# Kernel optimization log

Measured on AMD Instinct MI355X. Metric: run time of the kernel, lower is better.

## Reference

```python
import jax, jax.numpy as jnp
import numpy as np

B, H, SQ, SK, D = 2, 16, 2048, 2048, 128
SCALE = 0.20884964425119185
P_DROP = 0.125

def setup_inputs() -> dict:
    key = jax.random.key(0)
    k1, k2, k3 = jax.random.split(key, 3)
    x1 = jax.random.normal(k1, (B, H, SQ, D), dtype=jnp.float32)
    x2 = jax.random.normal(k2, (B, H, SK, D), dtype=jnp.float32)
    # inverted dropout mask: 0 with prob p, else 1/(1-p)
    keep = jax.random.uniform(k3, (B, H, SQ, SK)) >= P_DROP
    dropout_mask = keep.astype(jnp.float32) / (1.0 - P_DROP)
    return {"x1": x1, "x2": x2, "dropout_mask": dropout_mask}

def reference(x1, x2, dropout_mask):
    # scores: [B,H,Sq,Sk]
    scores = jnp.einsum('bhqd,bhkd->bhqk', x1, x2) * SCALE
    attn = jax.nn.softmax(scores, axis=-1)
    attn = attn * dropout_mask
    # output: [B,H,Sq,D]
    return jnp.einsum('bhqk,bhkd->bhqd', attn, x2)
```

## Files before the change

kernel.cpp:

```cpp
#include <hip/hip_runtime.h>
#include <hip/hip_bf16.h>

#define SQ 2048
#define SK 2048
#define DD 128
#define NBH 32
#define QBLK 128
#define KBLK 32
#define NKT (SK / KBLK)
#define SCALE 0.20884964425119185f
#define SCL2 (SCALE * 1.4426950408889634f)

typedef __attribute__((ext_vector_type(8))) short short8;
typedef __attribute__((ext_vector_type(4))) float f32x4;

#define KPITCH 272
#define VPITCH 80
#define K0OFF 0
#define K1OFF 8704
#define V0OFF 17408
#define V1OFF 27648
#define SMEM_BYTES 37888

static __device__ __forceinline__ unsigned int pk_bf16(float lo, float hi) {
    float2 f2; f2.x = lo; f2.y = hi;
    __hip_bfloat162 h = __float22bfloat162_rn(f2);
    union { __hip_bfloat162 h2; unsigned int u; } cv; cv.h2 = h;
    return cv.u;
}

#define SOFTMAX_PACK(PA, SA_, SB_, MCa, MCb, LPART)                            \
  { float p_[8];                                                               \
    p_[0] = __builtin_amdgcn_exp2f(SA_[0]*SCL2);                               \
    p_[1] = __builtin_amdgcn_exp2f(SA_[1]*SCL2);                               \
    p_[2] = __builtin_amdgcn_exp2f(SA_[2]*SCL2);                               \
    p_[3] = __builtin_amdgcn_exp2f(SA_[3]*SCL2);                               \
    p_[4] = __builtin_amdgcn_exp2f(SB_[0]*SCL2);                               \
    p_[5] = __builtin_amdgcn_exp2f(SB_[1]*SCL2);                               \
    p_[6] = __builtin_amdgcn_exp2f(SB_[2]*SCL2);                               \
    p_[7] = __builtin_amdgcn_exp2f(SB_[3]*SCL2);                               \
    LPART += ((p_[0]+p_[1]) + (p_[2]+p_[3])) + ((p_[4]+p_[5]) + (p_[6]+p_[7]));\
    p_[0]*=MCa.x; p_[1]*=MCa.y; p_[2]*=MCa.z; p_[3]*=MCa.w;                    \
    p_[4]*=MCb.x; p_[5]*=MCb.y; p_[6]*=MCb.z; p_[7]*=MCb.w;                    \
    unsigned int P0 = pk_bf16(p_[0],p_[1]), P1 = pk_bf16(p_[2],p_[3]);         \
    unsigned int P2 = pk_bf16(p_[4],p_[5]), P3 = pk_bf16(p_[6],p_[7]);         \
    unsigned int a0 = __shfl((int)P0, sA), a2 = __shfl((int)P2, sA);           \
    unsigned int b0 = __shfl((int)P1, sA), b2 = __shfl((int)P3, sA);           \
    unsigned int c0 = __shfl((int)P0, sB), c2 = __shfl((int)P2, sB);           \
    unsigned int d0 = __shfl((int)P1, sB), d2 = __shfl((int)P3, sB);           \
    union { unsigned int u[4]; short8 v; } pb_;                                \
    pb_.u[0] = hi ? a2 : a0; pb_.u[1] = hi ? b2 : b0;                          \
    pb_.u[2] = hi ? c2 : c0; pb_.u[3] = hi ? d2 : d0;                          \
    PA = pb_.v; }

#define STAGE_SYNC()                                                           \
    asm volatile("s_waitcnt lgkmcnt(0)" ::: "memory");                         \
    __builtin_amdgcn_sched_barrier(0);                                         \
    __builtin_amdgcn_s_barrier();                 \
    __builtin_amdgcn_sched_barrier(0);

#define COMPUTE_TILE(KOFF_, VOFF_, MC0, MC1, MC2, MC3)                         \
    f32x4 s00={0,0,0,0}, s01={0,0,0,0}, s10={0,0,0,0}, s11={0,0,0,0};          \
    __builtin_amdgcn_s_setprio(1);                                             \
    _Pragma("unroll")                                                          \
    for (int ks = 0; ks < 4; ++ks) {                                           \
      short8 ka0 = *(const short8*)(smem + (KOFF_) + (c)      * KPITCH + ks*64 + 16*g); \
      short8 ka1 = *(const short8*)(smem + (KOFF_) + (16 + c) * KPITCH + ks*64 + 16*g); \
      s00 = __builtin_amdgcn_mfma_f32_16x16x32_bf16(ka0, qf0[ks], s00, 0,0,0); \
      s01 = __builtin_amdgcn_mfma_f32_16x16x32_bf16(ka1, qf0[ks], s01, 0,0,0); \
      s10 = __builtin_amdgcn_mfma_f32_16x16x32_bf16(ka0, qf1[ks], s10, 0,0,0); \
      s11 = __builtin_amdgcn_mfma_f32_16x16x32_bf16(ka1, qf1[ks], s11, 0,0,0); \
    }                                                                          \
    __builtin_amdgcn_s_setprio(0);                                             \
    short8 pa0, pa1;                                                           \
    SOFTMAX_PACK(pa0, s00, s01, MC0, MC1, l0p)                                 \
    SOFTMAX_PACK(pa1, s10, s11, MC2, MC3, l1p)                                 \
    __builtin_amdgcn_s_setprio(1);                                             \
    _Pragma("unroll")                                                          \
    for (int d8 = 0; d8 < 8; ++d8) {                                           \
      short8 vv = *(const short8*)(smem + (VOFF_) + (d8*16 + c)*VPITCH + 16*g);\
      o0[d8] = __builtin_amdgcn_mfma_f32_16x16x32_bf16(pa0, vv, o0[d8], 0,0,0);\
      o1[d8] = __builtin_amdgcn_mfma_f32_16x16x32_bf16(pa1, vv, o1[d8], 0,0,0);\
    }                                                                          \
    __builtin_amdgcn_s_setprio(0);

#define BODY_BF(KC0,KC1,VC0,VC1, MC0,MC1,MC2,MC3,                              \
                KN0,KN1,VN0,VN1, MN0,MN1,MN2,MN3, KOFF_, VOFF_, KT)            \
  { const int kbn = ((KT) < NKT - 1) ? ((KT) + 1) * KBLK : (KT) * KBLK;        \
    KN0 = *(const short8*)(x2bb + (size_t)(kbn + kk)      * DD + kd0);         \
    KN1 = *(const short8*)(x2bb + (size_t)(kbn + kk + 16) * DD + kd0);         \
    VN0 = *(const short8*)(x2bb + (size_t)(kbn + 2*kp)     * DD + vdb);        \
    VN1 = *(const short8*)(x2bb + (size_t)(kbn + 2*kp + 1) * DD + vdb);        \
    MN0 = *(const float4*)(mq0 + kbn);                                         \
    MN1 = *(const float4*)(mq0 + kbn + 16);                                    \
    MN2 = *(const float4*)(mq1 + kbn);                                         \
    MN3 = *(const float4*)(mq1 + kbn + 16);                                    \
    *(short8*)(smem + (KOFF_) + (kk)      * KPITCH + 2*kd0) = KC0;             \
    *(short8*)(smem + (KOFF_) + (kk + 16) * KPITCH + 2*kd0) = KC1;             \
    { union { short8 s; unsigned int u[4]; } a_, b_;                           \
      a_.s = VC0; b_.s = VC1;                                                  \
      _Pragma("unroll")                                                        \
      for (int j = 0; j < 8; ++j) {                                            \
        unsigned int w = (j & 1)                                               \
            ? ((a_.u[j>>1] >> 16) | (b_.u[j>>1] & 0xffff0000u))                \
            : ((a_.u[j>>1] & 0xffffu) | (b_.u[j>>1] << 16));                   \
        *(unsigned int*)(smem + (VOFF_) + (vdb + j) * VPITCH + 4*kp) = w;      \
      } }                                                                      \
    STAGE_SYNC()                                                               \
    COMPUTE_TILE(KOFF_, VOFF_, MC0, MC1, MC2, MC3)                             \
  }

#define BODY_F32(KC0,KC1,KC2,KC3, VC0,VC1,VC2,VC3, MC0,MC1,MC2,MC3,            \
                 KN0,KN1,KN2,KN3, VN0,VN1,VN2,VN3, MN0,MN1,MN2,MN3,            \
                 KOFF_, VOFF_, KT)                                             \
  { const int kbn = ((KT) < NKT - 1) ? ((KT) + 1) * KBLK : (KT) * KBLK;        \
    KN0 = *(const float4*)(x2fb + (size_t)(kbn + kk)      * DD + kd0);         \
    KN1 = *(const float4*)(x2fb + (size_t)(kbn + kk)      * DD + kd0 + 4);     \
    KN2 = *(const float4*)(x2fb + (size_t)(kbn + kk + 16) * DD + kd0);         \
    KN3 = *(const float4*)(x2fb + (size_t)(kbn + kk + 16) * DD + kd0 + 4);     \
    VN0 = *(const float4*)(x2fb + (size_t)(kbn + 2*kp)     * DD + vdb);        \
    VN1 = *(const float4*)(x2fb + (size_t)(kbn + 2*kp)     * DD + vdb + 4);    \
    VN2 = *(const float4*)(x2fb + (size_t)(kbn + 2*kp + 1) * DD + vdb);        \
    VN3 = *(const float4*)(x2fb + (size_t)(kbn + 2*kp + 1) * DD + vdb + 4);    \
    MN0 = *(const float4*)(mq0 + kbn);                                         \
    MN1 = *(const float4*)(mq0 + kbn + 16);                                    \
    MN2 = *(const float4*)(mq1 + kbn);                                         \
    MN3 = *(const float4*)(mq1 + kbn + 16);                                    \
    { union { unsigned int u[4]; short8 s; } k0_, k1_;                         \
      k0_.u[0]=pk_bf16(KC0.x,KC0.y); k0_.u[1]=pk_bf16(KC0.z,KC0.w);            \
      k0_.u[2]=pk_bf16(KC1.x,KC1.y); k0_.u[3]=pk_bf16(KC1.z,KC1.w);            \
      k1_.u[0]=pk_bf16(KC2.x,KC2.y); k1_.u[1]=pk_bf16(KC2.z,KC2.w);            \
      k1_.u[2]=pk_bf16(KC3.x,KC3.y); k1_.u[3]=pk_bf16(KC3.z,KC3.w);            \
      *(short8*)(smem + (KOFF_) + (kk)      * KPITCH + 2*kd0) = k0_.s;         \
      *(short8*)(smem + (KOFF_) + (kk + 16) * KPITCH + 2*kd0) = k1_.s; }       \
    *(unsigned int*)(smem + (VOFF_) + (vdb+0)*VPITCH + 4*kp) = pk_bf16(VC0.x, VC2.x); \
    *(unsigned int*)(smem + (VOFF_) + (vdb+1)*VPITCH + 4*kp) = pk_bf16(VC0.y, VC2.y); \
    *(unsigned int*)(smem + (VOFF_) + (vdb+2)*VPITCH + 4*kp) = pk_bf16(VC0.z, VC2.z); \
    *(unsigned int*)(smem + (VOFF_) + (vdb+3)*VPITCH + 4*kp) = pk_bf16(VC0.w, VC2.w); \
    *(unsigned int*)(smem + (VOFF_) + (vdb+4)*VPITCH + 4*kp) = pk_bf16(VC1.x, VC3.x); \
    *(unsigned int*)(smem + (VOFF_) + (vdb+5)*VPITCH + 4*kp) = pk_bf16(VC1.y, VC3.y); \
    *(unsigned int*)(smem + (VOFF_) + (vdb+6)*VPITCH + 4*kp) = pk_bf16(VC1.z, VC3.z); \
    *(unsigned int*)(smem + (VOFF_) + (vdb+7)*VPITCH + 4*kp) = pk_bf16(VC1.w, VC3.w); \
    STAGE_SYNC()                                                               \
    COMPUTE_TILE(KOFF_, VOFF_, MC0, MC1, MC2, MC3)                             \
  }

#define KERNEL_PRE()                                                           \
    __shared__ __align__(16) unsigned char smem[SMEM_BYTES];                   \
    const int tid  = threadIdx.x;                                              \
    const int lane = tid & 63, wid = tid >> 6;                                 \
    const int c = lane & 15, g = lane >> 4;                                    \
    const int bid = blockIdx.x;                                                \
    const int swz = (bid & 7) * 64 + (bid >> 3);   \
    const int bh = swz >> 4;                                                   \
    const int qb = swz & 15;                                                   \
    const float* x1b = x1 + ((size_t)bh * SQ + (size_t)qb * QBLK) * DD;        \
    const float* mb  = mask + ((size_t)bh * SQ + (size_t)qb * QBLK) * SK;      \
    float*      outb = out + ((size_t)bh * SQ + (size_t)qb * QBLK) * DD;       \
    const int sA = c + ((g & 1) << 5);                                         \
    const int sB = sA + 16;                                                    \
    const bool hi = (g >= 2);                                                  \
    const int kk  = tid >> 4, kd0 = (tid & 15) * 8;                            \
    const int kp  = tid & 15, vdb = (tid >> 4) * 8;                            \
    const float* mq0 = mb + (size_t)(wid*16 + c) * SK + 4*g;                   \
    const float* mq1 = mq0 + (size_t)64 * SK;

#define KERNEL_QLOAD()                                                         \
    short8 qf0[4], qf1[4];                                                     \
    {  const float* q0r = x1b + (size_t)(wid*16 + c) * DD;                     \
       const float* q1r = q0r + (size_t)64 * DD;                               \
       _Pragma("unroll")                                                       \
       for (int ks = 0; ks < 4; ++ks) {                                        \
           float4 a = *(const float4*)(q0r + ks*32 + 8*g);                     \
           float4 b = *(const float4*)(q0r + ks*32 + 8*g + 4);                 \
           union { unsigned int u[4]; short8 s; } t;                           \
           t.u[0]=pk_bf16(a.x,a.y); t.u[1]=pk_bf16(a.z,a.w);                   \
           t.u[2]=pk_bf16(b.x,b.y); t.u[3]=pk_bf16(b.z,b.w);                   \
           qf0[ks]=t.s;                                                        \
           a = *(const float4*)(q1r + ks*32 + 8*g);                            \
           b = *(const float4*)(q1r + ks*32 + 8*g + 4);                        \
           t.u[0]=pk_bf16(a.x,a.y); t.u[1]=pk_bf16(a.z,a.w);                   \
           t.u[2]=pk_bf16(b.x,b.y); t.u[3]=pk_bf16(b.z,b.w);                   \
           qf1[ks]=t.s;                                                        \
       } }

#define KERNEL_EPILOGUE()                                                      \
    float l0 = l0p; l0 += __shfl_xor(l0, 16); l0 += __shfl_xor(l0, 32);        \
    float l1 = l1p; l1 += __shfl_xor(l1, 16); l1 += __shfl_xor(l1, 32);        \
    float il00 = 1.0f/__shfl(l0, 4*g+0), il01 = 1.0f/__shfl(l0, 4*g+1);        \
    float il02 = 1.0f/__shfl(l0, 4*g+2), il03 = 1.0f/__shfl(l0, 4*g+3);        \
    float il10 = 1.0f/__shfl(l1, 4*g+0), il11 = 1.0f/__shfl(l1, 4*g+1);        \
    float il12 = 1.0f/__shfl(l1, 4*g+2), il13 = 1.0f/__shfl(l1, 4*g+3);        \
    float* orow0 = outb + (size_t)(wid*16) * DD;                               \
    float* orow1 = outb + (size_t)(64 + wid*16) * DD;                          \
    _Pragma("unroll")                                                          \
    for (int d8 = 0; d8 < 8; ++d8) {                                           \
        orow0[(4*g + 0) * DD + d8*16 + c] = o0[d8][0] * il00;                  \
        orow0[(4*g + 1) * DD + d8*16 + c] = o0[d8][1] * il01;                  \
        orow0[(4*g + 2) * DD + d8*16 + c] = o0[d8][2] * il02;                  \
        orow0[(4*g + 3) * DD + d8*16 + c] = o0[d8][3] * il03;                  \
        orow1[(4*g + 0) * DD + d8*16 + c] = o1[d8][0] * il10;                  \
        orow1[(4*g + 1) * DD + d8*16 + c] = o1[d8][1] * il11;                  \
        orow1[(4*g + 2) * DD + d8*16 + c] = o1[d8][2] * il12;                  \
        orow1[(4*g + 3) * DD + d8*16 + c] = o1[d8][3] * il13;                  \
    }

__global__ __launch_bounds__(256) void cvt_x2(const float* __restrict__ src,
                                              unsigned short* __restrict__ dst,
                                              int n4) {
    int i = blockIdx.x * 256 + threadIdx.x;
    const int stride = gridDim.x * 256;
    for (; i < n4; i += stride) {
        float4 v = ((const float4*)src)[i];
        uint2 w; w.x = pk_bf16(v.x, v.y); w.y = pk_bf16(v.z, v.w);
        ((uint2*)dst)[i] = w;
    }
}

__global__ __launch_bounds__(256, 2) void fattn_bf16(
    const float* __restrict__ x1, const unsigned short* __restrict__ x2b,
    const float* __restrict__ mask, float* __restrict__ out)
{
    KERNEL_PRE()
    const unsigned short* x2bb = x2b + (size_t)bh * SK * DD;

    short8 kA0 = *(const short8*)(x2bb + (size_t)(kk)      * DD + kd0);
    short8 kA1 = *(const short8*)(x2bb + (size_t)(kk + 16) * DD + kd0);
    short8 vA0 = *(const short8*)(x2bb + (size_t)(2*kp)     * DD + vdb);
    short8 vA1 = *(const short8*)(x2bb + (size_t)(2*kp + 1) * DD + vdb);
    float4 mA0 = *(const float4*)(mq0);
    float4 mA1 = *(const float4*)(mq0 + 16);
    float4 mA2 = *(const float4*)(mq1);
    float4 mA3 = *(const float4*)(mq1 + 16);
    short8 kB0, kB1, vB0, vB1; float4 mB0, mB1, mB2, mB3;

    KERNEL_QLOAD()

    f32x4 o0[8] = {}, o1[8] = {};
    float l0p = 0.f, l1p = 0.f;

    for (int kt2 = 0; kt2 < NKT / 2; ++kt2) {
        BODY_BF(kA0,kA1,vA0,vA1, mA0,mA1,mA2,mA3,
                kB0,kB1,vB0,vB1, mB0,mB1,mB2,mB3, K0OFF, V0OFF, 2*kt2)
        BODY_BF(kB0,kB1,vB0,vB1, mB0,mB1,mB2,mB3,
                kA0,kA1,vA0,vA1, mA0,mA1,mA2,mA3, K1OFF, V1OFF, 2*kt2 + 1)
    }
    KERNEL_EPILOGUE()
}

__global__ __launch_bounds__(256, 2) void fattn_f32(
    const float* __restrict__ x1, const float* __restrict__ x2,
    const float* __restrict__ mask, float* __restrict__ out)
{
    KERNEL_PRE()
    const float* x2fb = x2 + (size_t)bh * SK * DD;

    float4 kA0 = *(const float4*)(x2fb + (size_t)(kk)      * DD + kd0);
    float4 kA1 = *(const float4*)(x2fb + (size_t)(kk)      * DD + kd0 + 4);
    float4 kA2 = *(const float4*)(x2fb + (size_t)(kk + 16) * DD + kd0);
    float4 kA3 = *(const float4*)(x2fb + (size_t)(kk + 16) * DD + kd0 + 4);
    float4 vA0 = *(const float4*)(x2fb + (size_t)(2*kp)     * DD + vdb);
    float4 vA1 = *(const float4*)(x2fb + (size_t)(2*kp)     * DD + vdb + 4);
    float4 vA2 = *(const float4*)(x2fb + (size_t)(2*kp + 1) * DD + vdb);
    float4 vA3 = *(const float4*)(x2fb + (size_t)(2*kp + 1) * DD + vdb + 4);
    float4 mA0 = *(const float4*)(mq0);
    float4 mA1 = *(const float4*)(mq0 + 16);
    float4 mA2 = *(const float4*)(mq1);
    float4 mA3 = *(const float4*)(mq1 + 16);
    float4 kB0,kB1,kB2,kB3, vB0,vB1,vB2,vB3, mB0,mB1,mB2,mB3;

    KERNEL_QLOAD()

    f32x4 o0[8] = {}, o1[8] = {};
    float l0p = 0.f, l1p = 0.f;

    for (int kt2 = 0; kt2 < NKT / 2; ++kt2) {
        BODY_F32(kA0,kA1,kA2,kA3, vA0,vA1,vA2,vA3, mA0,mA1,mA2,mA3,
                 kB0,kB1,kB2,kB3, vB0,vB1,vB2,vB3, mB0,mB1,mB2,mB3,
                 K0OFF, V0OFF, 2*kt2)
        BODY_F32(kB0,kB1,kB2,kB3, vB0,vB1,vB2,vB3, mB0,mB1,mB2,mB3,
                 kA0,kA1,kA2,kA3, vA0,vA1,vA2,vA3, mA0,mA1,mA2,mA3,
                 K1OFF, V1OFF, 2*kt2 + 1)
    }
    KERNEL_EPILOGUE()
}

extern "C" void kernel_launch(void* const* d_in, const int* in_sizes, int n_in,
                              void* d_out, int out_size, void* d_ws, size_t ws_size,
                              hipStream_t stream) {
    const float* x1   = (const float*)d_in[0];
    const float* x2   = (const float*)d_in[1];
    const float* mask = (const float*)d_in[2];
    float* out = (float*)d_out;
    const size_t need = (size_t)NBH * SK * DD * sizeof(unsigned short);
    if (ws_size >= need) {
        unsigned short* x2b = (unsigned short*)d_ws;
        cvt_x2<<<dim3(2048), dim3(256), 0, stream>>>(x2, x2b, NBH*SK*DD/4);
        fattn_bf16<<<dim3(NBH * (SQ / QBLK)), dim3(256), 0, stream>>>(x1, x2b, mask, out);
    } else {
        fattn_f32<<<dim3(NBH * (SQ / QBLK)), dim3(256), 0, stream>>>(x1, x2, mask, out);
    }
}
```

Before: 223.2 us.

## Restructure bf16 attention loop to compute current tile before staging next to LDS

The bf16 path now issues global loads for the next K/V tile, computes QK^T, softmax and PV from the already-staged LDS buffer, then writes the next tile into the alternate LDS buffer and synchronises once. This lets the global load latency overlap the MFMA work, and it issues dropout mask loads two tiles ahead. The first tile is staged in a prologue before the loop. The PV loop is also reordered to load two V fragments per iteration. The f32 fallback is rewritten to use a single buffer with two barriers per tile. Register pressure rises from holding prefetched data across the compute.

```diff
diff --git a/kernel.cpp b/kernel.cpp
--- a/kernel.cpp
+++ b/kernel.cpp
@@ -53,96 +53,69 @@
     pb_.u[2] = hi ? c2 : c0; pb_.u[3] = hi ? d2 : d0;                          \
     PA = pb_.v; }
 
-#define STAGE_SYNC()                                                           \
+#define BAR()                                                                  \
     asm volatile("s_waitcnt lgkmcnt(0)" ::: "memory");                         \
     __builtin_amdgcn_sched_barrier(0);                                         \
-    __builtin_amdgcn_s_barrier();                 \
+    __builtin_amdgcn_s_barrier();                                              \
     __builtin_amdgcn_sched_barrier(0);
 
-#define COMPUTE_TILE(KOFF_, VOFF_, MC0, MC1, MC2, MC3)                         \
+#define BODY_BF(KOFFc, VOFFc, KOFFn, VOFFn, MC0, MC1, MC2, MC3, KT)            \
+  {                                                                            \
+    const int kbn = (((KT) < NKT - 1) ? (KT) + 1 : (KT)) * KBLK;               \
+    const int kbm = (((KT) < NKT - 2) ? (KT) + 2 : (NKT - 1)) * KBLK;          \
+                   \
+    kC0 = *(const short8*)(x2bb + (size_t)(kbn + kk)      * DD + kd0);         \
+    kC1 = *(const short8*)(x2bb + (size_t)(kbn + kk + 16) * DD + kd0);         \
+    vC0 = *(const short8*)(x2bb + (size_t)(kbn + 2*kp)     * DD + vdb);        \
+    vC1 = *(const short8*)(x2bb + (size_t)(kbn + 2*kp + 1) * DD + vdb);        \
+                                                \
     f32x4 s00={0,0,0,0}, s01={0,0,0,0}, s10={0,0,0,0}, s11={0,0,0,0};          \
     __builtin_amdgcn_s_setprio(1);                                             \
     _Pragma("unroll")                                                          \
     for (int ks = 0; ks < 4; ++ks) {                                           \
-      short8 ka0 = *(const short8*)(smem + (KOFF_) + (c)      * KPITCH + ks*64 + 16*g); \
-      short8 ka1 = *(const short8*)(smem + (KOFF_) + (16 + c) * KPITCH + ks*64 + 16*g); \
+      short8 ka0 = *(const short8*)(smem + (KOFFc) + (c)      * KPITCH + ks*64 + 16*g); \
+      short8 ka1 = *(const short8*)(smem + (KOFFc) + (16 + c) * KPITCH + ks*64 + 16*g); \
       s00 = __builtin_amdgcn_mfma_f32_16x16x32_bf16(ka0, qf0[ks], s00, 0,0,0); \
       s01 = __builtin_amdgcn_mfma_f32_16x16x32_bf16(ka1, qf0[ks], s01, 0,0,0); \
       s10 = __builtin_amdgcn_mfma_f32_16x16x32_bf16(ka0, qf1[ks], s10, 0,0,0); \
       s11 = __builtin_amdgcn_mfma_f32_16x16x32_bf16(ka1, qf1[ks], s11, 0,0,0); \
     }                                                                          \
     __builtin_amdgcn_s_setprio(0);                                             \
+                                     \
     short8 pa0, pa1;                                                           \
     SOFTMAX_PACK(pa0, s00, s01, MC0, MC1, l0p)                                 \
     SOFTMAX_PACK(pa1, s10, s11, MC2, MC3, l1p)                                 \
+                                                \
     __builtin_amdgcn_s_setprio(1);                                             \
     _Pragma("unroll")                                                          \
-    for (int d8 = 0; d8 < 8; ++d8) {                                           \
-      short8 vv = *(const short8*)(smem + (VOFF_) + (d8*16 + c)*VPITCH + 16*g);\
-      o0[d8] = __builtin_amdgcn_mfma_f32_16x16x32_bf16(pa0, vv, o0[d8], 0,0,0);\
-      o1[d8] = __builtin_amdgcn_mfma_f32_16x16x32_bf16(pa1, vv, o1[d8], 0,0,0);\
+    for (int d4 = 0; d4 < 4; ++d4) {                                           \
+      short8 v0 = *(const short8*)(smem + (VOFFc) + ((2*d4)*16   + c)*VPITCH + 16*g); \
+      short8 v1 = *(const short8*)(smem + (VOFFc) + ((2*d4+1)*16 + c)*VPITCH + 16*g); \
+      o0[2*d4]   = __builtin_amdgcn_mfma_f32_16x16x32_bf16(pa0, v0, o0[2*d4],   0,0,0); \
+      o1[2*d4]   = __builtin_amdgcn_mfma_f32_16x16x32_bf16(pa1, v0, o1[2*d4],   0,0,0); \
+      o0[2*d4+1] = __builtin_amdgcn_mfma_f32_16x16x32_bf16(pa0, v1, o0[2*d4+1], 0,0,0); \
+      o1[2*d4+1] = __builtin_amdgcn_mfma_f32_16x16x32_bf16(pa1, v1, o1[2*d4+1], 0,0,0); \
     }                                                                          \
-    __builtin_amdgcn_s_setprio(0);
-
-#define BODY_BF(KC0,KC1,VC0,VC1, MC0,MC1,MC2,MC3,                              \
-                KN0,KN1,VN0,VN1, MN0,MN1,MN2,MN3, KOFF_, VOFF_, KT)            \
-  { const int kbn = ((KT) < NKT - 1) ? ((KT) + 1) * KBLK : (KT) * KBLK;        \
-    KN0 = *(const short8*)(x2bb + (size_t)(kbn + kk)      * DD + kd0);         \
-    KN1 = *(const short8*)(x2bb + (size_t)(kbn + kk + 16) * DD + kd0);         \
-    VN0 = *(const short8*)(x2bb + (size_t)(kbn + 2*kp)     * DD + vdb);        \
-    VN1 = *(const short8*)(x2bb + (size_t)(kbn + 2*kp + 1) * DD + vdb);        \
-    MN0 = *(const float4*)(mq0 + kbn);                                         \
-    MN1 = *(const float4*)(mq0 + kbn + 16);                                    \
-    MN2 = *(const float4*)(mq1 + kbn);                                         \
-    MN3 = *(const float4*)(mq1 + kbn + 16);                                    \
-    *(short8*)(smem + (KOFF_) + (kk)      * KPITCH + 2*kd0) = KC0;             \
-    *(short8*)(smem + (KOFF_) + (kk + 16) * KPITCH + 2*kd0) = KC1;             \
+    __builtin_amdgcn_s_setprio(0);                                             \
+     \
+    *(short8*)(smem + (KOFFn) + (kk)      * KPITCH + 2*kd0) = kC0;             \
+    *(short8*)(smem + (KOFFn) + (kk + 16) * KPITCH + 2*kd0) = kC1;             \
     { union { short8 s; unsigned int u[4]; } a_, b_;                           \
-      a_.s = VC0; b_.s = VC1;                                                  \
+      a_.s = vC0; b_.s = vC1;                                                  \
       _Pragma("unroll")                                                        \
       for (int j = 0; j < 8; ++j) {                                            \
         unsigned int w = (j & 1)                                               \
             ? ((a_.u[j>>1] >> 16) | (b_.u[j>>1] & 0xffff0000u))                \
             : ((a_.u[j>>1] & 0xffffu) | (b_.u[j>>1] << 16));                   \
-        *(unsigned int*)(smem + (VOFF_) + (vdb + j) * VPITCH + 4*kp) = w;      \
+        *(unsigned int*)(smem + (VOFFn) + (vdb + j) * VPITCH + 4*kp) = w;      \
       } }                                                                      \
-    STAGE_SYNC()                                                               \
-    COMPUTE_TILE(KOFF_, VOFF_, MC0, MC1, MC2, MC3)                             \
-  }
-
-#define BODY_F32(KC0,KC1,KC2,KC3, VC0,VC1,VC2,VC3, MC0,MC1,MC2,MC3,            \
-                 KN0,KN1,KN2,KN3, VN0,VN1,VN2,VN3, MN0,MN1,MN2,MN3,            \
-                 KOFF_, VOFF_, KT)                                             \
-  { const int kbn = ((KT) < NKT - 1) ? ((KT) + 1) * KBLK : (KT) * KBLK;        \
-    KN0 = *(const float4*)(x2fb + (size_t)(kbn + kk)      * DD + kd0);         \
-    KN1 = *(const float4*)(x2fb + (size_t)(kbn + kk)      * DD + kd0 + 4);     \
-    KN2 = *(const float4*)(x2fb + (size_t)(kbn + kk + 16) * DD + kd0);         \
-    KN3 = *(const float4*)(x2fb + (size_t)(kbn + kk + 16) * DD + kd0 + 4);     \
-    VN0 = *(const float4*)(x2fb + (size_t)(kbn + 2*kp)     * DD + vdb);        \
-    VN1 = *(const float4*)(x2fb + (size_t)(kbn + 2*kp)     * DD + vdb + 4);    \
-    VN2 = *(const float4*)(x2fb + (size_t)(kbn + 2*kp + 1) * DD + vdb);        \
-    VN3 = *(const float4*)(x2fb + (size_t)(kbn + 2*kp + 1) * DD + vdb + 4);    \
-    MN0 = *(const float4*)(mq0 + kbn);                                         \
-    MN1 = *(const float4*)(mq0 + kbn + 16);                                    \
-    MN2 = *(const float4*)(mq1 + kbn);                                         \
-    MN3 = *(const float4*)(mq1 + kbn + 16);                                    \
-    { union { unsigned int u[4]; short8 s; } k0_, k1_;                         \
-      k0_.u[0]=pk_bf16(KC0.x,KC0.y); k0_.u[1]=pk_bf16(KC0.z,KC0.w);            \
-      k0_.u[2]=pk_bf16(KC1.x,KC1.y); k0_.u[3]=pk_bf16(KC1.z,KC1.w);            \
-      k1_.u[0]=pk_bf16(KC2.x,KC2.y); k1_.u[1]=pk_bf16(KC2.z,KC2.w);            \
-      k1_.u[2]=pk_bf16(KC3.x,KC3.y); k1_.u[3]=pk_bf16(KC3.z,KC3.w);            \
-      *(short8*)(smem + (KOFF_) + (kk)      * KPITCH + 2*kd0) = k0_.s;         \
-      *(short8*)(smem + (KOFF_) + (kk + 16) * KPITCH + 2*kd0) = k1_.s; }       \
-    *(unsigned int*)(smem + (VOFF_) + (vdb+0)*VPITCH + 4*kp) = pk_bf16(VC0.x, VC2.x); \
-    *(unsigned int*)(smem + (VOFF_) + (vdb+1)*VPITCH + 4*kp) = pk_bf16(VC0.y, VC2.y); \
-    *(unsigned int*)(smem + (VOFF_) + (vdb+2)*VPITCH + 4*kp) = pk_bf16(VC0.z, VC2.z); \
-    *(unsigned int*)(smem + (VOFF_) + (vdb+3)*VPITCH + 4*kp) = pk_bf16(VC0.w, VC2.w); \
-    *(unsigned int*)(smem + (VOFF_) + (vdb+4)*VPITCH + 4*kp) = pk_bf16(VC1.x, VC3.x); \
-    *(unsigned int*)(smem + (VOFF_) + (vdb+5)*VPITCH + 4*kp) = pk_bf16(VC1.y, VC3.y); \
-    *(unsigned int*)(smem + (VOFF_) + (vdb+6)*VPITCH + 4*kp) = pk_bf16(VC1.z, VC3.z); \
-    *(unsigned int*)(smem + (VOFF_) + (vdb+7)*VPITCH + 4*kp) = pk_bf16(VC1.w, VC3.w); \
-    STAGE_SYNC()                                                               \
-    COMPUTE_TILE(KOFF_, VOFF_, MC0, MC1, MC2, MC3)                             \
+    \
+    MC0 = *(const float4*)(mq0 + kbm);                                         \
+    MC1 = *(const float4*)(mq0 + kbm + 16);                                    \
+    MC2 = *(const float4*)(mq1 + kbm);                                         \
+    MC3 = *(const float4*)(mq1 + kbm + 16);                                    \
+                                       \
+    BAR()                                                                      \
   }
 
 #define KERNEL_PRE()                                                           \
@@ -224,29 +197,102 @@
     KERNEL_PRE()
     const unsigned short* x2bb = x2b + (size_t)bh * SK * DD;
 
-    short8 kA0 = *(const short8*)(x2bb + (size_t)(kk)      * DD + kd0);
-    short8 kA1 = *(const short8*)(x2bb + (size_t)(kk + 16) * DD + kd0);
-    short8 vA0 = *(const short8*)(x2bb + (size_t)(2*kp)     * DD + vdb);
-    short8 vA1 = *(const short8*)(x2bb + (size_t)(2*kp + 1) * DD + vdb);
+    short8 kC0 = *(const short8*)(x2bb + (size_t)(kk)      * DD + kd0);
+    short8 kC1 = *(const short8*)(x2bb + (size_t)(kk + 16) * DD + kd0);
+    short8 vC0 = *(const short8*)(x2bb + (size_t)(2*kp)     * DD + vdb);
+    short8 vC1 = *(const short8*)(x2bb + (size_t)(2*kp + 1) * DD + vdb);
     float4 mA0 = *(const float4*)(mq0);
     float4 mA1 = *(const float4*)(mq0 + 16);
     float4 mA2 = *(const float4*)(mq1);
     float4 mA3 = *(const float4*)(mq1 + 16);
-    short8 kB0, kB1, vB0, vB1; float4 mB0, mB1, mB2, mB3;
+    float4 mB0 = *(const float4*)(mq0 + KBLK);
+    float4 mB1 = *(const float4*)(mq0 + KBLK + 16);
+    float4 mB2 = *(const float4*)(mq1 + KBLK);
+    float4 mB3 = *(const float4*)(mq1 + KBLK + 16);
 
     KERNEL_QLOAD()
+
+    *(short8*)(smem + K0OFF + (kk)      * KPITCH + 2*kd0) = kC0;
+    *(short8*)(smem + K0OFF + (kk + 16) * KPITCH + 2*kd0) = kC1;
+    { union { short8 s; unsigned int u[4]; } a_, b_;
+      a_.s = vC0; b_.s = vC1;
+#pragma unroll
+      for (int j = 0; j < 8; ++j) {
+        unsigned int w = (j & 1)
+            ? ((a_.u[j>>1] >> 16) | (b_.u[j>>1] & 0xffff0000u))
+            : ((a_.u[j>>1] & 0xffffu) | (b_.u[j>>1] << 16));
+        *(unsigned int*)(smem + V0OFF + (vdb + j) * VPITCH + 4*kp) = w;
+      } }
+    BAR()
 
     f32x4 o0[8] = {}, o1[8] = {};
     float l0p = 0.f, l1p = 0.f;
 
     for (int kt2 = 0; kt2 < NKT / 2; ++kt2) {
-        BODY_BF(kA0,kA1,vA0,vA1, mA0,mA1,mA2,mA3,
-                kB0,kB1,vB0,vB1, mB0,mB1,mB2,mB3, K0OFF, V0OFF, 2*kt2)
-        BODY_BF(kB0,kB1,vB0,vB1, mB0,mB1,mB2,mB3,
-                kA0,kA1,vA0,vA1, mA0,mA1,mA2,mA3, K1OFF, V1OFF, 2*kt2 + 1)
+        BODY_BF(K0OFF, V0OFF, K1OFF, V1OFF, mA0, mA1, mA2, mA3, 2*kt2)
+        BODY_BF(K1OFF, V1OFF, K0OFF, V0OFF, mB0, mB1, mB2, mB3, 2*kt2 + 1)
     }
     KERNEL_EPILOGUE()
 }
+
+#define F32_SYNC()                                                             \
+    asm volatile("s_waitcnt lgkmcnt(0)" ::: "memory");                         \
+    __builtin_amdgcn_sched_barrier(0);                                         \
+    __builtin_amdgcn_s_barrier();                                              \
+    __builtin_amdgcn_sched_barrier(0);
+
+#define BODY_F32(KC0,KC1,KC2,KC3, VC0,VC1,VC2,VC3, MC0,MC1,MC2,MC3,            \
+                 KN0,KN1,KN2,KN3, VN0,VN1,VN2,VN3, MN0,MN1,MN2,MN3, KT)        \
+  { const int kbn = ((KT) < NKT - 1) ? ((KT) + 1) * KBLK : (KT) * KBLK;        \
+    KN0 = *(const float4*)(x2fb + (size_t)(kbn + kk)      * DD + kd0);         \
+    KN1 = *(const float4*)(x2fb + (size_t)(kbn + kk)      * DD + kd0 + 4);     \
+    KN2 = *(const float4*)(x2fb + (size_t)(kbn + kk + 16) * DD + kd0);         \
+    KN3 = *(const float4*)(x2fb + (size_t)(kbn + kk + 16) * DD + kd0 + 4);     \
+    VN0 = *(const float4*)(x2fb + (size_t)(kbn + 2*kp)     * DD + vdb);        \
+    VN1 = *(const float4*)(x2fb + (size_t)(kbn + 2*kp)     * DD + vdb + 4);    \
+    VN2 = *(const float4*)(x2fb + (size_t)(kbn + 2*kp + 1) * DD + vdb);        \
+    VN3 = *(const float4*)(x2fb + (size_t)(kbn + 2*kp + 1) * DD + vdb + 4);    \
+    MN0 = *(const float4*)(mq0 + kbn);                                         \
+    MN1 = *(const float4*)(mq0 + kbn + 16);                                    \
+    MN2 = *(const float4*)(mq1 + kbn);                                         \
+    MN3 = *(const float4*)(mq1 + kbn + 16);                                    \
+    { union { unsigned int u[4]; short8 s; } k0_, k1_;                         \
+      k0_.u[0]=pk_bf16(KC0.x,KC0.y); k0_.u[1]=pk_bf16(KC0.z,KC0.w);            \
+      k0_.u[2]=pk_bf16(KC1.x,KC1.y); k0_.u[3]=pk_bf16(KC1.z,KC1.w);            \
+      k1_.u[0]=pk_bf16(KC2.x,KC2.y); k1_.u[1]=pk_bf16(KC2.z,KC2.w);            \
+      k1_.u[2]=pk_bf16(KC3.x,KC3.y); k1_.u[3]=pk_bf16(KC3.z,KC3.w);            \
+      *(short8*)(smem + K0OFF + (kk)      * KPITCH + 2*kd0) = k0_.s;           \
+      *(short8*)(smem + K0OFF + (kk + 16) * KPITCH + 2*kd0) = k1_.s; }         \
+    *(unsigned int*)(smem + V0OFF + (vdb+0)*VPITCH + 4*kp) = pk_bf16(VC0.x, VC2.x); \
+    *(unsigned int*)(smem + V0OFF + (vdb+1)*VPITCH + 4*kp) = pk_bf16(VC0.y, VC2.y); \
+    *(unsigned int*)(smem + V0OFF + (vdb+2)*VPITCH + 4*kp) = pk_bf16(VC0.z, VC2.z); \
+    *(unsigned int*)(smem + V0OFF + (vdb+3)*VPITCH + 4*kp) = pk_bf16(VC0.w, VC2.w); \
+    *(unsigned int*)(smem + V0OFF + (vdb+4)*VPITCH + 4*kp) = pk_bf16(VC1.x, VC3.x); \
+    *(unsigned int*)(smem + V0OFF + (vdb+5)*VPITCH + 4*kp) = pk_bf16(VC1.y, VC3.y); \
+    *(unsigned int*)(smem + V0OFF + (vdb+6)*VPITCH + 4*kp) = pk_bf16(VC1.z, VC3.z); \
+    *(unsigned int*)(smem + V0OFF + (vdb+7)*VPITCH + 4*kp) = pk_bf16(VC1.w, VC3.w); \
+    F32_SYNC()                                                                 \
+    f32x4 s00={0,0,0,0}, s01={0,0,0,0}, s10={0,0,0,0}, s11={0,0,0,0};          \
+    _Pragma("unroll")                                                          \
+    for (int ks = 0; ks < 4; ++ks) {                                           \
+      short8 ka0 = *(const short8*)(smem + K0OFF + (c)      * KPITCH + ks*64 + 16*g); \
+      short8 ka1 = *(const short8*)(smem + K0OFF + (16 + c) * KPITCH + ks*64 + 16*g); \
+      s00 = __builtin_amdgcn_mfma_f32_16x16x32_bf16(ka0, qf0[ks], s00, 0,0,0); \
+      s01 = __builtin_amdgcn_mfma_f32_16x16x32_bf16(ka1, qf0[ks], s01, 0,0,0); \
+      s10 = __builtin_amdgcn_mfma_f32_16x16x32_bf16(ka0, qf1[ks], s10, 0,0,0); \
+      s11 = __builtin_amdgcn_mfma_f32_16x16x32_bf16(ka1, qf1[ks], s11, 0,0,0); \
+    }                                                                          \
+    short8 pa0, pa1;                                                           \
+    SOFTMAX_PACK(pa0, s00, s01, MC0, MC1, l0p)                                 \
+    SOFTMAX_PACK(pa1, s10, s11, MC2, MC3, l1p)                                 \
+    _Pragma("unroll")                                                          \
+    for (int d8 = 0; d8 < 8; ++d8) {                                           \
+      short8 vv = *(const short8*)(smem + V0OFF + (d8*16 + c)*VPITCH + 16*g);  \
+      o0[d8] = __builtin_amdgcn_mfma_f32_16x16x32_bf16(pa0, vv, o0[d8], 0,0,0);\
+      o1[d8] = __builtin_amdgcn_mfma_f32_16x16x32_bf16(pa1, vv, o1[d8], 0,0,0);\
+    }                                                                          \
+    F32_SYNC()                                                                 \
+  }
 
 __global__ __launch_bounds__(256, 2) void fattn_f32(
     const float* __restrict__ x1, const float* __restrict__ x2,
@@ -276,11 +322,9 @@
 
     for (int kt2 = 0; kt2 < NKT / 2; ++kt2) {
         BODY_F32(kA0,kA1,kA2,kA3, vA0,vA1,vA2,vA3, mA0,mA1,mA2,mA3,
-                 kB0,kB1,kB2,kB3, vB0,vB1,vB2,vB3, mB0,mB1,mB2,mB3,
-                 K0OFF, V0OFF, 2*kt2)
+                 kB0,kB1,kB2,kB3, vB0,vB1,vB2,vB3, mB0,mB1,mB2,mB3, 2*kt2)
         BODY_F32(kB0,kB1,kB2,kB3, vB0,vB1,vB2,vB3, mB0,mB1,mB2,mB3,
-                 kA0,kA1,kA2,kA3, vA0,vA1,vA2,vA3, mA0,mA1,mA2,mA3,
-                 K1OFF, V1OFF, 2*kt2 + 1)
+                 kA0,kA1,kA2,kA3, vA0,vA1,vA2,vA3, mA0,mA1,mA2,mA3, 2*kt2 + 1)
     }
     KERNEL_EPILOGUE()
 }
```

Result: faster. 210.5 us (-5.7%).

## Halve query tile to 64 rows, single-buffer LDS, raise occupancy

Applied to the files above, without the earlier changes.

Each block now processes 64 query rows instead of 128, so every wave owns one 16-row slice. The double-buffered K/V LDS staging becomes a single buffer with a second barrier after compute, which halves shared memory. Launch bounds rise to 4 blocks per CU for the bf16 kernel and 3 for the f32 fallback, and the grid doubles. The goal is more occupancy and better latency hiding of the mask stream. In exchange, K/V is reloaded from global memory twice as often per query row, each tile costs an extra barrier, and each wave does less MFMA work per K/V tile.

```diff
diff --git a/kernel.cpp b/kernel.cpp
--- a/kernel.cpp
+++ b/kernel.cpp
@@ -5,7 +5,7 @@
 #define SK 2048
 #define DD 128
 #define NBH 32
-#define QBLK 128
+#define QBLK 64
 #define KBLK 32
 #define NKT (SK / KBLK)
 #define SCALE 0.20884964425119185f
@@ -16,11 +16,8 @@
 
 #define KPITCH 272
 #define VPITCH 80
-#define K0OFF 0
-#define K1OFF 8704
-#define V0OFF 17408
-#define V1OFF 27648
-#define SMEM_BYTES 37888
+#define VOFF 8704
+#define SMEM_BYTES 18944
 
 static __device__ __forceinline__ unsigned int pk_bf16(float lo, float hi) {
     float2 f2; f2.x = lo; f2.y = hi;
@@ -53,39 +50,13 @@
     pb_.u[2] = hi ? c2 : c0; pb_.u[3] = hi ? d2 : d0;                          \
     PA = pb_.v; }
 
-#define STAGE_SYNC()                                                           \
+#define BAR()                                                                  \
     asm volatile("s_waitcnt lgkmcnt(0)" ::: "memory");                         \
     __builtin_amdgcn_sched_barrier(0);                                         \
-    __builtin_amdgcn_s_barrier();                 \
+    __builtin_amdgcn_s_barrier();                                              \
     __builtin_amdgcn_sched_barrier(0);
 
-#define COMPUTE_TILE(KOFF_, VOFF_, MC0, MC1, MC2, MC3)                         \
-    f32x4 s00={0,0,0,0}, s01={0,0,0,0}, s10={0,0,0,0}, s11={0,0,0,0};          \
-    __builtin_amdgcn_s_setprio(1);                                             \
-    _Pragma("unroll")                                                          \
-    for (int ks = 0; ks < 4; ++ks) {                                           \
-      short8 ka0 = *(const short8*)(smem + (KOFF_) + (c)      * KPITCH + ks*64 + 16*g); \
-      short8 ka1 = *(const short8*)(smem + (KOFF_) + (16 + c) * KPITCH + ks*64 + 16*g); \
-      s00 = __builtin_amdgcn_mfma_f32_16x16x32_bf16(ka0, qf0[ks], s00, 0,0,0); \
-      s01 = __builtin_amdgcn_mfma_f32_16x16x32_bf16(ka1, qf0[ks], s01, 0,0,0); \
-      s10 = __builtin_amdgcn_mfma_f32_16x16x32_bf16(ka0, qf1[ks], s10, 0,0,0); \
-      s11 = __builtin_amdgcn_mfma_f32_16x16x32_bf16(ka1, qf1[ks], s11, 0,0,0); \
-    }                                                                          \
-    __builtin_amdgcn_s_setprio(0);                                             \
-    short8 pa0, pa1;                                                           \
-    SOFTMAX_PACK(pa0, s00, s01, MC0, MC1, l0p)                                 \
-    SOFTMAX_PACK(pa1, s10, s11, MC2, MC3, l1p)                                 \
-    __builtin_amdgcn_s_setprio(1);                                             \
-    _Pragma("unroll")                                                          \
-    for (int d8 = 0; d8 < 8; ++d8) {                                           \
-      short8 vv = *(const short8*)(smem + (VOFF_) + (d8*16 + c)*VPITCH + 16*g);\
-      o0[d8] = __builtin_amdgcn_mfma_f32_16x16x32_bf16(pa0, vv, o0[d8], 0,0,0);\
-      o1[d8] = __builtin_amdgcn_mfma_f32_16x16x32_bf16(pa1, vv, o1[d8], 0,0,0);\
-    }                                                                          \
-    __builtin_amdgcn_s_setprio(0);
-
-#define BODY_BF(KC0,KC1,VC0,VC1, MC0,MC1,MC2,MC3,                              \
-                KN0,KN1,VN0,VN1, MN0,MN1,MN2,MN3, KOFF_, VOFF_, KT)            \
+#define BODY_BF(KC0,KC1,VC0,VC1, MC0,MC1, KN0,KN1,VN0,VN1, MN0,MN1, KT)        \
   { const int kbn = ((KT) < NKT - 1) ? ((KT) + 1) * KBLK : (KT) * KBLK;        \
     KN0 = *(const short8*)(x2bb + (size_t)(kbn + kk)      * DD + kd0);         \
     KN1 = *(const short8*)(x2bb + (size_t)(kbn + kk + 16) * DD + kd0);         \
@@ -93,10 +64,8 @@
     VN1 = *(const short8*)(x2bb + (size_t)(kbn + 2*kp + 1) * DD + vdb);        \
     MN0 = *(const float4*)(mq0 + kbn);                                         \
     MN1 = *(const float4*)(mq0 + kbn + 16);                                    \
-    MN2 = *(const float4*)(mq1 + kbn);                                         \
-    MN3 = *(const float4*)(mq1 + kbn + 16);                                    \
-    *(short8*)(smem + (KOFF_) + (kk)      * KPITCH + 2*kd0) = KC0;             \
-    *(short8*)(smem + (KOFF_) + (kk + 16) * KPITCH + 2*kd0) = KC1;             \
+    *(short8*)(smem + (kk)      * KPITCH + 2*kd0) = KC0;                       \
+    *(short8*)(smem + (kk + 16) * KPITCH + 2*kd0) = KC1;                       \
     { union { short8 s; unsigned int u[4]; } a_, b_;                           \
       a_.s = VC0; b_.s = VC1;                                                  \
       _Pragma("unroll")                                                        \
@@ -104,15 +73,117 @@
         unsigned int w = (j & 1)                                               \
             ? ((a_.u[j>>1] >> 16) | (b_.u[j>>1] & 0xffff0000u))                \
             : ((a_.u[j>>1] & 0xffffu) | (b_.u[j>>1] << 16));                   \
-        *(unsigned int*)(smem + (VOFF_) + (vdb + j) * VPITCH + 4*kp) = w;      \
+        *(unsigned int*)(smem + VOFF + (vdb + j) * VPITCH + 4*kp) = w;         \
       } }                                                                      \
-    STAGE_SYNC()                                                               \
-    COMPUTE_TILE(KOFF_, VOFF_, MC0, MC1, MC2, MC3)                             \
+    BAR()                                                                      \
+    f32x4 s00={0,0,0,0}, s01={0,0,0,0};                                        \
+    __builtin_amdgcn_s_setprio(1);                                             \
+    _Pragma("unroll")                                                          \
+    for (int ks = 0; ks < 4; ++ks) {                                           \
+      short8 ka0 = *(const short8*)(smem + (c)      * KPITCH + ks*64 + 16*g);  \
+      short8 ka1 = *(const short8*)(smem + (16 + c) * KPITCH + ks*64 + 16*g);  \
+      s00 = __builtin_amdgcn_mfma_f32_16x16x32_bf16(ka0, qf[ks], s00, 0,0,0);  \
+      s01 = __builtin_amdgcn_mfma_f32_16x16x32_bf16(ka1, qf[ks], s01, 0,0,0);  \
+    }                                                                          \
+    __builtin_amdgcn_s_setprio(0);                                             \
+    short8 pa;                                                                 \
+    SOFTMAX_PACK(pa, s00, s01, MC0, MC1, lp)                                   \
+    __builtin_amdgcn_s_setprio(1);                                             \
+    _Pragma("unroll")                                                          \
+    for (int d8 = 0; d8 < 8; ++d8) {                                           \
+      short8 vv = *(const short8*)(smem + VOFF + (d8*16 + c)*VPITCH + 16*g);   \
+      o[d8] = __builtin_amdgcn_mfma_f32_16x16x32_bf16(pa, vv, o[d8], 0,0,0);   \
+    }                                                                          \
+    __builtin_amdgcn_s_setprio(0);                                             \
+    BAR()                                                                      \
   }
 
-#define BODY_F32(KC0,KC1,KC2,KC3, VC0,VC1,VC2,VC3, MC0,MC1,MC2,MC3,            \
-                 KN0,KN1,KN2,KN3, VN0,VN1,VN2,VN3, MN0,MN1,MN2,MN3,            \
-                 KOFF_, VOFF_, KT)                                             \
+#define KERNEL_PRE()                                                           \
+    __shared__ __align__(16) unsigned char smem[SMEM_BYTES];                   \
+    const int tid  = threadIdx.x;                                              \
+    const int lane = tid & 63, wid = tid >> 6;                                 \
+    const int c = lane & 15, g = lane >> 4;                                    \
+    const int bid = blockIdx.x;                                                \
+    const int swz = (bid & 7) * 128 + (bid >> 3);  \
+    const int bh = swz >> 5;                                                   \
+    const int qb = swz & 31;                                                   \
+    const float* x1b = x1 + ((size_t)bh * SQ + (size_t)qb * QBLK) * DD;        \
+    const float* mb  = mask + ((size_t)bh * SQ + (size_t)qb * QBLK) * SK;      \
+    float*      outb = out + ((size_t)bh * SQ + (size_t)qb * QBLK) * DD;       \
+    const int sA = c + ((g & 1) << 5);                                         \
+    const int sB = sA + 16;                                                    \
+    const bool hi = (g >= 2);                                                  \
+    const int kk  = tid >> 4, kd0 = (tid & 15) * 8;                            \
+    const int kp  = tid & 15, vdb = (tid >> 4) * 8;                            \
+    const float* mq0 = mb + (size_t)(wid*16 + c) * SK + 4*g;
+
+#define KERNEL_QLOAD()                                                         \
+    short8 qf[4];                                                              \
+    {  const float* q0r = x1b + (size_t)(wid*16 + c) * DD;                     \
+       _Pragma("unroll")                                                       \
+       for (int ks = 0; ks < 4; ++ks) {                                        \
+           float4 a = *(const float4*)(q0r + ks*32 + 8*g);                     \
+           float4 b = *(const float4*)(q0r + ks*32 + 8*g + 4);                 \
+           union { unsigned int u[4]; short8 s; } t;                           \
+           t.u[0]=pk_bf16(a.x,a.y); t.u[1]=pk_bf16(a.z,a.w);                   \
+           t.u[2]=pk_bf16(b.x,b.y); t.u[3]=pk_bf16(b.z,b.w);                   \
+           qf[ks]=t.s;                                                         \
+       } }
+
+#define KERNEL_EPILOGUE()                                                      \
+    float l = lp; l += __shfl_xor(l, 16); l += __shfl_xor(l, 32);              \
+    float il0 = 1.0f/__shfl(l, 4*g+0), il1 = 1.0f/__shfl(l, 4*g+1);            \
+    float il2 = 1.0f/__shfl(l, 4*g+2), il3 = 1.0f/__shfl(l, 4*g+3);            \
+    float* orow = outb + (size_t)(wid*16) * DD;                                \
+    _Pragma("unroll")                                                          \
+    for (int d8 = 0; d8 < 8; ++d8) {                                           \
+        orow[(4*g + 0) * DD + d8*16 + c] = o[d8][0] * il0;                     \
+        orow[(4*g + 1) * DD + d8*16 + c] = o[d8][1] * il1;                     \
+        orow[(4*g + 2) * DD + d8*16 + c] = o[d8][2] * il2;                     \
+        orow[(4*g + 3) * DD + d8*16 + c] = o[d8][3] * il3;                     \
+    }
+
+__global__ __launch_bounds__(256) void cvt_x2(const float* __restrict__ src,
+                                              unsigned short* __restrict__ dst,
+                                              int n4) {
+    int i = blockIdx.x * 256 + threadIdx.x;
+    const int stride = gridDim.x * 256;
+    for (; i < n4; i += stride) {
+        float4 v = ((const float4*)src)[i];
+        uint2 w; w.x = pk_bf16(v.x, v.y); w.y = pk_bf16(v.z, v.w);
+        ((uint2*)dst)[i] = w;
+    }
+}
+
+__global__ __launch_bounds__(256, 4) void fattn_bf16(
+    const float* __restrict__ x1, const unsigned short* __restrict__ x2b,
+    const float* __restrict__ mask, float* __restrict__ out)
+{
+    KERNEL_PRE()
+    const unsigned short* x2bb = x2b + (size_t)bh * SK * DD;
+
+    short8 kA0 = *(const short8*)(x2bb + (size_t)(kk)      * DD + kd0);
+    short8 kA1 = *(const short8*)(x2bb + (size_t)(kk + 16) * DD + kd0);
+    short8 vA0 = *(const short8*)(x2bb + (size_t)(2*kp)     * DD + vdb);
+    short8 vA1 = *(const short8*)(x2bb + (size_t)(2*kp + 1) * DD + vdb);
+    float4 mA0 = *(const float4*)(mq0);
+    float4 mA1 = *(const float4*)(mq0 + 16);
+    short8 kB0, kB1, vB0, vB1; float4 mB0, mB1;
+
+    KERNEL_QLOAD()
+
+    f32x4 o[8] = {};
+    float lp = 0.f;
+
+    for (int kt2 = 0; kt2 < NKT / 2; ++kt2) {
+        BODY_BF(kA0,kA1,vA0,vA1, mA0,mA1, kB0,kB1,vB0,vB1, mB0,mB1, 2*kt2)
+        BODY_BF(kB0,kB1,vB0,vB1, mB0,mB1, kA0,kA1,vA0,vA1, mA0,mA1, 2*kt2 + 1)
+    }
+    KERNEL_EPILOGUE()
+}
+
+#define BODY_F32(KC0,KC1,KC2,KC3, VC0,VC1,VC2,VC3, MC0,MC1,                    \
+                 KN0,KN1,KN2,KN3, VN0,VN1,VN2,VN3, MN0,MN1, KT)                \
   { const int kbn = ((KT) < NKT - 1) ? ((KT) + 1) * KBLK : (KT) * KBLK;        \
     KN0 = *(const float4*)(x2fb + (size_t)(kbn + kk)      * DD + kd0);         \
     KN1 = *(const float4*)(x2fb + (size_t)(kbn + kk)      * DD + kd0 + 4);     \
@@ -124,131 +195,41 @@
     VN3 = *(const float4*)(x2fb + (size_t)(kbn + 2*kp + 1) * DD + vdb + 4);    \
     MN0 = *(const float4*)(mq0 + kbn);                                         \
     MN1 = *(const float4*)(mq0 + kbn + 16);                                    \
-    MN2 = *(const float4*)(mq1 + kbn);                                         \
-    MN3 = *(const float4*)(mq1 + kbn + 16);                                    \
     { union { unsigned int u[4]; short8 s; } k0_, k1_;                         \
       k0_.u[0]=pk_bf16(KC0.x,KC0.y); k0_.u[1]=pk_bf16(KC0.z,KC0.w);            \
       k0_.u[2]=pk_bf16(KC1.x,KC1.y); k0_.u[3]=pk_bf16(KC1.z,KC1.w);            \
       k1_.u[0]=pk_bf16(KC2.x,KC2.y); k1_.u[1]=pk_bf16(KC2.z,KC2.w);            \
       k1_.u[2]=pk_bf16(KC3.x,KC3.y); k1_.u[3]=pk_bf16(KC3.z,KC3.w);            \
-      *(short8*)(smem + (KOFF_) + (kk)      * KPITCH + 2*kd0) = k0_.s;         \
-      *(short8*)(smem + (KOFF_) + (kk + 16) * KPITCH + 2*kd0) = k1_.s; }       \
-    *(unsigned int*)(smem + (VOFF_) + (vdb+0)*VPITCH + 4*kp) = pk_bf16(VC0.x, VC2.x); \
-    *(unsigned int*)(smem + (VOFF_) + (vdb+1)*VPITCH + 4*kp) = pk_bf16(VC0.y, VC2.y); \
-    *(unsigned int*)(smem + (VOFF_) + (vdb+2)*VPITCH + 4*kp) = pk_bf16(VC0.z, VC2.z); \
-    *(unsigned int*)(smem + (VOFF_) + (vdb+3)*VPITCH + 4*kp) = pk_bf16(VC0.w, VC2.w); \
-    *(unsigned int*)(smem + (VOFF_) + (vdb+4)*VPITCH + 4*kp) = pk_bf16(VC1.x, VC3.x); \
-    *(unsigned int*)(smem + (VOFF_) + (vdb+5)*VPITCH + 4*kp) = pk_bf16(VC1.y, VC3.y); \
-    *(unsigned int*)(smem + (VOFF_) + (vdb+6)*VPITCH + 4*kp) = pk_bf16(VC1.z, VC3.z); \
-    *(unsigned int*)(smem + (VOFF_) + (vdb+7)*VPITCH + 4*kp) = pk_bf16(VC1.w, VC3.w); \
-    STAGE_SYNC()                                                               \
-    COMPUTE_TILE(KOFF_, VOFF_, MC0, MC1, MC2, MC3)                             \
+      *(short8*)(smem + (kk)      * KPITCH + 2*kd0) = k0_.s;                   \
+      *(short8*)(smem + (kk + 16) * KPITCH + 2*kd0) = k1_.s; }                 \
+    *(unsigned int*)(smem + VOFF + (vdb+0)*VPITCH + 4*kp) = pk_bf16(VC0.x, VC2.x); \
+    *(unsigned int*)(smem + VOFF + (vdb+1)*VPITCH + 4*kp) = pk_bf16(VC0.y, VC2.y); \
+    *(unsigned int*)(smem + VOFF + (vdb+2)*VPITCH + 4*kp) = pk_bf16(VC0.z, VC2.z); \
+    *(unsigned int*)(smem + VOFF + (vdb+3)*VPITCH + 4*kp) = pk_bf16(VC0.w, VC2.w); \
+    *(unsigned int*)(smem + VOFF + (vdb+4)*VPITCH + 4*kp) = pk_bf16(VC1.x, VC3.x); \
+    *(unsigned int*)(smem + VOFF + (vdb+5)*VPITCH + 4*kp) = pk_bf16(VC1.y, VC3.y); \
+    *(unsigned int*)(smem + VOFF + (vdb+6)*VPITCH + 4*kp) = pk_bf16(VC1.z, VC3.z); \
+    *(unsigned int*)(smem + VOFF + (vdb+7)*VPITCH + 4*kp) = pk_bf16(VC1.w, VC3.w); \
+    BAR()                                                                      \
+    f32x4 s00={0,0,0,0}, s01={0,0,0,0};                                        \
+    _Pragma("unroll")                                                          \
+    for (int ks = 0; ks < 4; ++ks) {                                           \
+      short8 ka0 = *(const short8*)(smem + (c)      * KPITCH + ks*64 + 16*g);  \
+      short8 ka1 = *(const short8*)(smem + (16 + c) * KPITCH + ks*64 + 16*g);  \
+      s00 = __builtin_amdgcn_mfma_f32_16x16x32_bf16(ka0, qf[ks], s00, 0,0,0);  \
+      s01 = __builtin_amdgcn_mfma_f32_16x16x32_bf16(ka1, qf[ks], s01, 0,0,0);  \
+    }                                                                          \
+    short8 pa;                                                                 \
+    SOFTMAX_PACK(pa, s00, s01, MC0, MC1, lp)                                   \
+    _Pragma("unroll")                                                          \
+    for (int d8 = 0; d8 < 8; ++d8) {                                           \
+      short8 vv = *(const short8*)(smem + VOFF + (d8*16 + c)*VPITCH + 16*g);   \
+      o[d8] = __builtin_amdgcn_mfma_f32_16x16x32_bf16(pa, vv, o[d8], 0,0,0);   \
+    }                                                                          \
+    BAR()                                                                      \
   }
 
-#define KERNEL_PRE()                                                           \
-    __shared__ __align__(16) unsigned char smem[SMEM_BYTES];                   \
-    const int tid  = threadIdx.x;                                              \
-    const int lane = tid & 63, wid = tid >> 6;                                 \
-    const int c = lane & 15, g = lane >> 4;                                    \
-    const int bid = blockIdx.x;                                                \
-    const int swz = (bid & 7) * 64 + (bid >> 3);   \
-    const int bh = swz >> 4;                                                   \
-    const int qb = swz & 15;                                                   \
-    const float* x1b = x1 + ((size_t)bh * SQ + (size_t)qb * QBLK) * DD;        \
-    const float* mb  = mask + ((size_t)bh * SQ + (size_t)qb * QBLK) * SK;      \
-    float*      outb = out + ((size_t)bh * SQ + (size_t)qb * QBLK) * DD;       \
-    const int sA = c + ((g & 1) << 5);                                         \
-    const int sB = sA + 16;                                                    \
-    const bool hi = (g >= 2);                                                  \
-    const int kk  = tid >> 4, kd0 = (tid & 15) * 8;                            \
-    const int kp  = tid & 15, vdb = (tid >> 4) * 8;                            \
-    const float* mq0 = mb + (size_t)(wid*16 + c) * SK + 4*g;                   \
-    const float* mq1 = mq0 + (size_t)64 * SK;
-
-#define KERNEL_QLOAD()                                                         \
-    short8 qf0[4], qf1[4];                                                     \
-    {  const float* q0r = x1b + (size_t)(wid*16 + c) * DD;                     \
-       const float* q1r = q0r + (size_t)64 * DD;                               \
-       _Pragma("unroll")                                                       \
-       for (int ks = 0; ks < 4; ++ks) {                                        \
-           float4 a = *(const float4*)(q0r + ks*32 + 8*g);                     \
-           float4 b = *(const float4*)(q0r + ks*32 + 8*g + 4);                 \
-           union { unsigned int u[4]; short8 s; } t;                           \
-           t.u[0]=pk_bf16(a.x,a.y); t.u[1]=pk_bf16(a.z,a.w);                   \
-           t.u[2]=pk_bf16(b.x,b.y); t.u[3]=pk_bf16(b.z,b.w);                   \
-           qf0[ks]=t.s;                                                        \
-           a = *(const float4*)(q1r + ks*32 + 8*g);                            \
-           b = *(const float4*)(q1r + ks*32 + 8*g + 4);                        \
-           t.u[0]=pk_bf16(a.x,a.y); t.u[1]=pk_bf16(a.z,a.w);                   \
-           t.u[2]=pk_bf16(b.x,b.y); t.u[3]=pk_bf16(b.z,b.w);                   \
-           qf1[ks]=t.s;                                                        \
-       } }
-
-#define KERNEL_EPILOGUE()                                                      \
-    float l0 = l0p; l0 += __shfl_xor(l0, 16); l0 += __shfl_xor(l0, 32);        \
-    float l1 = l1p; l1 += __shfl_xor(l1, 16); l1 += __shfl_xor(l1, 32);        \
-    float il00 = 1.0f/__shfl(l0, 4*g+0), il01 = 1.0f/__shfl(l0, 4*g+1);        \
-    float il02 = 1.0f/__shfl(l0, 4*g+2), il03 = 1.0f/__shfl(l0, 4*g+3);        \
-    float il10 = 1.0f/__shfl(l1, 4*g+0), il11 = 1.0f/__shfl(l1, 4*g+1);        \
-    float il12 = 1.0f/__shfl(l1, 4*g+2), il13 = 1.0f/__shfl(l1, 4*g+3);        \
-    float* orow0 = outb + (size_t)(wid*16) * DD;                               \
-    float* orow1 = outb + (size_t)(64 + wid*16) * DD;                          \
-    _Pragma("unroll")                                                          \
-    for (int d8 = 0; d8 < 8; ++d8) {                                           \
-        orow0[(4*g + 0) * DD + d8*16 + c] = o0[d8][0] * il00;                  \
-        orow0[(4*g + 1) * DD + d8*16 + c] = o0[d8][1] * il01;                  \
-        orow0[(4*g + 2) * DD + d8*16 + c] = o0[d8][2] * il02;                  \
-        orow0[(4*g + 3) * DD + d8*16 + c] = o0[d8][3] * il03;                  \
-        orow1[(4*g + 0) * DD + d8*16 + c] = o1[d8][0] * il10;                  \
-        orow1[(4*g + 1) * DD + d8*16 + c] = o1[d8][1] * il11;                  \
-        orow1[(4*g + 2) * DD + d8*16 + c] = o1[d8][2] * il12;                  \
-        orow1[(4*g + 3) * DD + d8*16 + c] = o1[d8][3] * il13;                  \
-    }
-
-__global__ __launch_bounds__(256) void cvt_x2(const float* __restrict__ src,
-                                              unsigned short* __restrict__ dst,
-                                              int n4) {
-    int i = blockIdx.x * 256 + threadIdx.x;
-    const int stride = gridDim.x * 256;
-    for (; i < n4; i += stride) {
-        float4 v = ((const float4*)src)[i];
-        uint2 w; w.x = pk_bf16(v.x, v.y); w.y = pk_bf16(v.z, v.w);
-        ((uint2*)dst)[i] = w;
-    }
-}
-
-__global__ __launch_bounds__(256, 2) void fattn_bf16(
-    const float* __restrict__ x1, const unsigned short* __restrict__ x2b,
-    const float* __restrict__ mask, float* __restrict__ out)
-{
-    KERNEL_PRE()
-    const unsigned short* x2bb = x2b + (size_t)bh * SK * DD;
-
-    short8 kA0 = *(const short8*)(x2bb + (size_t)(kk)      * DD + kd0);
-    short8 kA1 = *(const short8*)(x2bb + (size_t)(kk + 16) * DD + kd0);
-    short8 vA0 = *(const short8*)(x2bb + (size_t)(2*kp)     * DD + vdb);
-    short8 vA1 = *(const short8*)(x2bb + (size_t)(2*kp + 1) * DD + vdb);
-    float4 mA0 = *(const float4*)(mq0);
-    float4 mA1 = *(const float4*)(mq0 + 16);
-    float4 mA2 = *(const float4*)(mq1);
-    float4 mA3 = *(const float4*)(mq1 + 16);
-    short8 kB0, kB1, vB0, vB1; float4 mB0, mB1, mB2, mB3;
-
-    KERNEL_QLOAD()
-
-    f32x4 o0[8] = {}, o1[8] = {};
-    float l0p = 0.f, l1p = 0.f;
-
-    for (int kt2 = 0; kt2 < NKT / 2; ++kt2) {
-        BODY_BF(kA0,kA1,vA0,vA1, mA0,mA1,mA2,mA3,
-                kB0,kB1,vB0,vB1, mB0,mB1,mB2,mB3, K0OFF, V0OFF, 2*kt2)
-        BODY_BF(kB0,kB1,vB0,vB1, mB0,mB1,mB2,mB3,
-                kA0,kA1,vA0,vA1, mA0,mA1,mA2,mA3, K1OFF, V1OFF, 2*kt2 + 1)
-    }
-    KERNEL_EPILOGUE()
-}
-
-__global__ __launch_bounds__(256, 2) void fattn_f32(
+__global__ __launch_bounds__(256, 3) void fattn_f32(
     const float* __restrict__ x1, const float* __restrict__ x2,
     const float* __restrict__ mask, float* __restrict__ out)
 {
@@ -265,22 +246,18 @@
     float4 vA3 = *(const float4*)(x2fb + (size_t)(2*kp + 1) * DD + vdb + 4);
     float4 mA0 = *(const float4*)(mq0);
     float4 mA1 = *(const float4*)(mq0 + 16);
-    float4 mA2 = *(const float4*)(mq1);
-    float4 mA3 = *(const float4*)(mq1 + 16);
-    float4 kB0,kB1,kB2,kB3, vB0,vB1,vB2,vB3, mB0,mB1,mB2,mB3;
+    float4 kB0,kB1,kB2,kB3, vB0,vB1,vB2,vB3, mB0,mB1;
 
     KERNEL_QLOAD()
 
-    f32x4 o0[8] = {}, o1[8] = {};
-    float l0p = 0.f, l1p = 0.f;
+    f32x4 o[8] = {};
+    float lp = 0.f;
 
     for (int kt2 = 0; kt2 < NKT / 2; ++kt2) {
-        BODY_F32(kA0,kA1,kA2,kA3, vA0,vA1,vA2,vA3, mA0,mA1,mA2,mA3,
-                 kB0,kB1,kB2,kB3, vB0,vB1,vB2,vB3, mB0,mB1,mB2,mB3,
-                 K0OFF, V0OFF, 2*kt2)
-        BODY_F32(kB0,kB1,kB2,kB3, vB0,vB1,vB2,vB3, mB0,mB1,mB2,mB3,
-                 kA0,kA1,kA2,kA3, vA0,vA1,vA2,vA3, mA0,mA1,mA2,mA3,
-                 K1OFF, V1OFF, 2*kt2 + 1)
+        BODY_F32(kA0,kA1,kA2,kA3, vA0,vA1,vA2,vA3, mA0,mA1,
+                 kB0,kB1,kB2,kB3, vB0,vB1,vB2,vB3, mB0,mB1, 2*kt2)
+        BODY_F32(kB0,kB1,kB2,kB3, vB0,vB1,vB2,vB3, mB0,mB1,
+                 kA0,kA1,kA2,kA3, vA0,vA1,vA2,vA3, mA0,mA1, 2*kt2 + 1)
     }
     KERNEL_EPILOGUE()
 }
```

New measurement: 184.6 us. 1.21x faster.
